# Kernel optimization log

Hardware: AMD Instinct MI355X
Metric: run time of the kernel (lower is better)

## Reference

```python
import jax, jax.numpy as jnp
import numpy as np

B, NQ, NM = 8, 1024, 2048
DIM, HEADS, DHEAD, MLP = 512, 8, 64, 2048
INNER = HEADS * DHEAD
EPS = 1e-5


def layernorm(x, g, b):
    mu = jnp.mean(x, axis=-1, keepdims=True)
    var = jnp.mean(jnp.square(x - mu), axis=-1, keepdims=True)
    return (x - mu) * jax.lax.rsqrt(var + EPS) * g + b


def mha(q_in, k_in, v_in, wq, wk, wv, wo, bo, g, b):
    Bq, Nq, _ = q_in.shape
    Nk = k_in.shape[1]
    q = (q_in @ wq).reshape(Bq, Nq, HEADS, DHEAD)
    k = (k_in @ wk).reshape(Bq, Nk, HEADS, DHEAD)
    v = (v_in @ wv).reshape(Bq, Nk, HEADS, DHEAD)
    scale = DHEAD ** -0.5
    dots = jnp.einsum('bqhd,bkhd->bhqk', q, k) * scale
    attn = jax.nn.softmax(dots, axis=-1)
    out = jnp.einsum('bhqk,bkhd->bqhd', attn, v).reshape(Bq, Nq, INNER)
    out = out @ wo + bo
    return layernorm(out, g, b) + q_in


def ffn(x, w1, b1, w2, b2, g, b):
    h = jax.nn.relu(x @ w1 + b1)
    return layernorm(h @ w2 + b2, g, b) + x


def _mha_params(key, s=0.02):
    ks = jax.random.split(key, 4)
    return dict(
        wq=jax.random.normal(ks[0], (DIM, INNER), jnp.float32) * s,
        wk=jax.random.normal(ks[1], (DIM, INNER), jnp.float32) * s,
        wv=jax.random.normal(ks[2], (DIM, INNER), jnp.float32) * s,
        wo=jax.random.normal(ks[3], (INNER, DIM), jnp.float32) * s,
        bo=jnp.zeros((DIM,), jnp.float32),
        g=jnp.ones((DIM,), jnp.float32),
        b=jnp.zeros((DIM,), jnp.float32),
    )


def _ffn_params(key, s=0.02):
    ks = jax.random.split(key, 2)
    return dict(
        w1=jax.random.normal(ks[0], (DIM, MLP), jnp.float32) * s,
        b1=jnp.zeros((MLP,), jnp.float32),
        w2=jax.random.normal(ks[1], (MLP, DIM), jnp.float32) * s,
        b2=jnp.zeros((DIM,), jnp.float32),
        g=jnp.ones((DIM,), jnp.float32),
        b=jnp.zeros((DIM,), jnp.float32),
    )


def setup_inputs() -> dict:
    key = jax.random.key(0)
    ks = jax.random.split(key, 8)
    inp = {
        'tgt': jax.random.normal(ks[0], (B, NQ, DIM), jnp.float32),
        'memory': jax.random.normal(ks[1], (B, NM, DIM), jnp.float32),
        'pos': jax.random.normal(ks[2], (B, NM, DIM), jnp.float32),
        'query_pos': jax.random.normal(ks[3], (B, NQ, DIM), jnp.float32),
    }
    a0 = _mha_params(ks[4]); f0 = _ffn_params(ks[5])
    a1 = _mha_params(ks[6]); f1 = _ffn_params(ks[7])
    for name, d in (('a0', a0), ('f0', f0), ('a1', a1), ('f1', f1)):
        for k, v in d.items():
            inp[f'{name}_{k}'] = v
    return inp


def reference(tgt, memory, pos, query_pos,
              a0_wq, a0_wk, a0_wv, a0_wo, a0_bo, a0_g, a0_b,
              f0_w1, f0_b1, f0_w2, f0_b2, f0_g, f0_b,
              a1_wq, a1_wk, a1_wv, a1_wo, a1_bo, a1_g, a1_b,
              f1_w1, f1_b1, f1_w2, f1_b2, f1_g, f1_b):
    # self-attention: q=k=tgt+query_pos, v=tgt
    q0 = tgt + query_pos
    x = mha(q0, q0, tgt, a0_wq, a0_wk, a0_wv, a0_wo, a0_bo, a0_g, a0_b)
    x = ffn(x, f0_w1, f0_b1, f0_w2, f0_b2, f0_g, f0_b)
    # cross-attention: q=x+query_pos, k=memory+pos, v=memory
    q = x + query_pos
    k = memory + pos
    x = mha(q, k, memory, a1_wq, a1_wk, a1_wv, a1_wo, a1_bo, a1_g, a1_b)
    x = ffn(x, f1_w1, f1_b1, f1_w2, f1_b2, f1_g, f1_b)
    return x
```

## Files before the change

### kernel.cpp

```cpp
#include <hip/hip_runtime.h>
#include <stdint.h>
#include <stddef.h>

typedef __attribute__((ext_vector_type(8))) short short8;
typedef __attribute__((ext_vector_type(4))) short short4v;
typedef __attribute__((ext_vector_type(4))) float floatx4;

#define DEV __device__ __forceinline__

DEV float bf2f(short s) {
    union { float f; uint32_t u; } v;
    v.u = ((uint32_t)(uint16_t)s) << 16;
    return v.f;
}
DEV short f2bf(float f) {
    union { float f; uint32_t u; } v;
    v.f = f;
    uint32_t u = v.u + 0x7FFFu + ((v.u >> 16) & 1u);
    return (short)(u >> 16);
}
DEV short f2bf_tr(float f) {
    union { float f; uint32_t u; } v;
    v.f = f;
    return (short)(v.u >> 16);
}

template<int BIAS, int RELU, int OUTBF>
__global__ __launch_bounds__(256) void gemm_bt(
    const short* __restrict__ A, const short* __restrict__ Bt,
    const float* __restrict__ bias, void* __restrict__ Cout,
    int M, int N, int K)
{
    __shared__ short Alds[2][128 * 32];
    __shared__ short Blds[2][128 * 32];
    const int tid  = threadIdx.x;
    const int wave = tid >> 6, lane = tid & 63;
    const int g = lane >> 4, li = lane & 15;

    const int gx = gridDim.x;
    int flat = blockIdx.y * gx + blockIdx.x;
    const int nwg = gx * gridDim.y;
    flat = (flat & 7) * (nwg >> 3) + (flat >> 3);
    const long bm = (long)(flat % gx) * 128;
    const long bn = (long)(flat / gx) * 128;

    const int wr = (wave >> 1) * 64;
    const int wc = (wave & 1) * 64;
    const int srow = wave * 32 + (lane >> 2);
    const int scol = (lane & 3) * 8;
    const short* Ap = A + (bm + srow) * (long)K + scol;
    const short* Bp = Bt + (bn + srow) * (long)K + scol;

    auto STAGE = [&](int buf, int k0) {
        __builtin_amdgcn_global_load_lds(
            (const __attribute__((address_space(1))) void*)(Ap + k0),
            (__attribute__((address_space(3))) void*)(&Alds[buf][wave * 1024]), 16, 0, 0);
        __builtin_amdgcn_global_load_lds(
            (const __attribute__((address_space(1))) void*)(Ap + (long)16 * K + k0),
            (__attribute__((address_space(3))) void*)(&Alds[buf][wave * 1024 + 512]), 16, 0, 0);
        __builtin_amdgcn_global_load_lds(
            (const __attribute__((address_space(1))) void*)(Bp + k0),
            (__attribute__((address_space(3))) void*)(&Blds[buf][wave * 1024]), 16, 0, 0);
        __builtin_amdgcn_global_load_lds(
            (const __attribute__((address_space(1))) void*)(Bp + (long)16 * K + k0),
            (__attribute__((address_space(3))) void*)(&Blds[buf][wave * 1024 + 512]), 16, 0, 0);
    };

    floatx4 acc[4][4];
#pragma unroll
    for (int i = 0; i < 4; i++)
#pragma unroll
        for (int j = 0; j < 4; j++) acc[i][j] = (floatx4){0.f, 0.f, 0.f, 0.f};

    STAGE(0, 0);
    __syncthreads();
    int cur = 0;
    for (int k0 = 0; k0 < K; k0 += 32) {
        if (k0 + 32 < K) STAGE(cur ^ 1, k0 + 32);

        short8 af[4], bfr[4];
#pragma unroll
        for (int mi = 0; mi < 4; mi++)
            af[mi] = *(const short8*)(&Alds[cur][(wr + mi * 16 + li) * 32 + g * 8]);
#pragma unroll
        for (int ni = 0; ni < 4; ni++)
            bfr[ni] = *(const short8*)(&Blds[cur][(wc + ni * 16 + li) * 32 + g * 8]);
#pragma unroll
        for (int mi = 0; mi < 4; mi++)
#pragma unroll
            for (int ni = 0; ni < 4; ni++)
                acc[mi][ni] = __builtin_amdgcn_mfma_f32_16x16x32_bf16(
                    af[mi], bfr[ni], acc[mi][ni], 0, 0, 0);

        __syncthreads();
        cur ^= 1;
    }

    float* Cf = (float*)Cout;
    short* Cb = (short*)Cout;
#pragma unroll
    for (int mi = 0; mi < 4; mi++) {
#pragma unroll
        for (int ni = 0; ni < 4; ni++) {
            const long col = bn + wc + ni * 16 + li;
            const float bv = BIAS ? bias[col] : 0.f;
#pragma unroll
            for (int i = 0; i < 4; i++) {
                const long row = bm + wr + mi * 16 + g * 4 + i;
                float v = acc[mi][ni][i] + bv;
                if (RELU) v = fmaxf(v, 0.f);
                if (OUTBF) Cb[row * N + col] = f2bf(v);
                else       Cf[row * N + col] = v;
            }
        }
    }
}

__global__ __launch_bounds__(256) void gemm_bt2(
    const short* __restrict__ A0, const short* __restrict__ A1,
    const short* __restrict__ Bt, short* __restrict__ Cout,
    int M, int N, int K, int nsplit)
{
    __shared__ short Alds[2][128 * 32];
    __shared__ short Blds[2][128 * 32];
    const int tid  = threadIdx.x;
    const int wave = tid >> 6, lane = tid & 63;
    const int g = lane >> 4, li = lane & 15;

    const int gx = gridDim.x;
    int flat = blockIdx.y * gx + blockIdx.x;
    const int nwg = gx * gridDim.y;
    flat = (flat & 7) * (nwg >> 3) + (flat >> 3);
    const long bm = (long)(flat % gx) * 128;
    const long bn = (long)(flat / gx) * 128;

    const int wr = (wave >> 1) * 64;
    const int wc = (wave & 1) * 64;
    const int srow = wave * 32 + (lane >> 2);
    const int scol = (lane & 3) * 8;
    const short* A = (bn < nsplit) ? A0 : A1;
    const short* Ap = A + (bm + srow) * (long)K + scol;
    const short* Bp = Bt + (bn + srow) * (long)K + scol;

    auto STAGE = [&](int buf, int k0) {
        __builtin_amdgcn_global_load_lds(
            (const __attribute__((address_space(1))) void*)(Ap + k0),
            (__attribute__((address_space(3))) void*)(&Alds[buf][wave * 1024]), 16, 0, 0);
        __builtin_amdgcn_global_load_lds(
            (const __attribute__((address_space(1))) void*)(Ap + (long)16 * K + k0),
            (__attribute__((address_space(3))) void*)(&Alds[buf][wave * 1024 + 512]), 16, 0, 0);
        __builtin_amdgcn_global_load_lds(
            (const __attribute__((address_space(1))) void*)(Bp + k0),
            (__attribute__((address_space(3))) void*)(&Blds[buf][wave * 1024]), 16, 0, 0);
        __builtin_amdgcn_global_load_lds(
            (const __attribute__((address_space(1))) void*)(Bp + (long)16 * K + k0),
            (__attribute__((address_space(3))) void*)(&Blds[buf][wave * 1024 + 512]), 16, 0, 0);
    };

    floatx4 acc[4][4];
#pragma unroll
    for (int i = 0; i < 4; i++)
#pragma unroll
        for (int j = 0; j < 4; j++) acc[i][j] = (floatx4){0.f, 0.f, 0.f, 0.f};

    STAGE(0, 0);
    __syncthreads();
    int cur = 0;
    for (int k0 = 0; k0 < K; k0 += 32) {
        if (k0 + 32 < K) STAGE(cur ^ 1, k0 + 32);
        short8 af[4], bfr[4];
#pragma unroll
        for (int mi = 0; mi < 4; mi++)
            af[mi] = *(const short8*)(&Alds[cur][(wr + mi * 16 + li) * 32 + g * 8]);
#pragma unroll
        for (int ni = 0; ni < 4; ni++)
            bfr[ni] = *(const short8*)(&Blds[cur][(wc + ni * 16 + li) * 32 + g * 8]);
#pragma unroll
        for (int mi = 0; mi < 4; mi++)
#pragma unroll
            for (int ni = 0; ni < 4; ni++)
                acc[mi][ni] = __builtin_amdgcn_mfma_f32_16x16x32_bf16(
                    af[mi], bfr[ni], acc[mi][ni], 0, 0, 0);
        __syncthreads();
        cur ^= 1;
    }

#pragma unroll
    for (int mi = 0; mi < 4; mi++)
#pragma unroll
        for (int ni = 0; ni < 4; ni++) {
            const long col = bn + wc + ni * 16 + li;
#pragma unroll
            for (int i = 0; i < 4; i++) {
                const long row = bm + wr + mi * 16 + g * 4 + i;
                Cout[row * N + col] = f2bf(acc[mi][ni][i]);
            }
        }
}

template<int BIAS>
__global__ __launch_bounds__(256) void gemm_bt_sk(
    const short* __restrict__ A, const short* __restrict__ Bt,
    const float* __restrict__ bias, float* __restrict__ Cout,
    int M, int N, int K)
{
    __shared__ short Alds[2][128 * 32];
    __shared__ short Blds[2][128 * 32];
    const int tid  = threadIdx.x;
    const int wave = tid >> 6, lane = tid & 63;
    const int g = lane >> 4, li = lane & 15;
    const int z = blockIdx.z;
    const int Kh = K >> 1;

    const int gx = gridDim.x;
    int flat = blockIdx.y * gx + blockIdx.x;
    const int nwg = gx * gridDim.y;
    flat = (flat & 7) * (nwg >> 3) + (flat >> 3);
    const long bm = (long)(flat % gx) * 128;
    const long bn = (long)(flat / gx) * 128;

    const int wr = (wave >> 1) * 64;
    const int wc = (wave & 1) * 64;
    const int srow = wave * 32 + (lane >> 2);
    const int scol = (lane & 3) * 8;
    const short* Ap = A + (bm + srow) * (long)K + scol + (long)z * Kh;
    const short* Bp = Bt + (bn + srow) * (long)K + scol + (long)z * Kh;
    float* C = Cout + (long)z * M * N;

    auto STAGE = [&](int buf, int k0) {
        __builtin_amdgcn_global_load_lds(
            (const __attribute__((address_space(1))) void*)(Ap + k0),
            (__attribute__((address_space(3))) void*)(&Alds[buf][wave * 1024]), 16, 0, 0);
        __builtin_amdgcn_global_load_lds(
            (const __attribute__((address_space(1))) void*)(Ap + (long)16 * K + k0),
            (__attribute__((address_space(3))) void*)(&Alds[buf][wave * 1024 + 512]), 16, 0, 0);
        __builtin_amdgcn_global_load_lds(
            (const __attribute__((address_space(1))) void*)(Bp + k0),
            (__attribute__((address_space(3))) void*)(&Blds[buf][wave * 1024]), 16, 0, 0);
        __builtin_amdgcn_global_load_lds(
            (const __attribute__((address_space(1))) void*)(Bp + (long)16 * K + k0),
            (__attribute__((address_space(3))) void*)(&Blds[buf][wave * 1024 + 512]), 16, 0, 0);
    };

    floatx4 acc[4][4];
#pragma unroll
    for (int i = 0; i < 4; i++)
#pragma unroll
        for (int j = 0; j < 4; j++) acc[i][j] = (floatx4){0.f, 0.f, 0.f, 0.f};

    STAGE(0, 0);
    __syncthreads();
    int cur = 0;
    for (int k0 = 0; k0 < Kh; k0 += 32) {
        if (k0 + 32 < Kh) STAGE(cur ^ 1, k0 + 32);
        short8 af[4], bfr[4];
#pragma unroll
        for (int mi = 0; mi < 4; mi++)
            af[mi] = *(const short8*)(&Alds[cur][(wr + mi * 16 + li) * 32 + g * 8]);
#pragma unroll
        for (int ni = 0; ni < 4; ni++)
            bfr[ni] = *(const short8*)(&Blds[cur][(wc + ni * 16 + li) * 32 + g * 8]);
#pragma unroll
        for (int mi = 0; mi < 4; mi++)
#pragma unroll
            for (int ni = 0; ni < 4; ni++)
                acc[mi][ni] = __builtin_amdgcn_mfma_f32_16x16x32_bf16(
                    af[mi], bfr[ni], acc[mi][ni], 0, 0, 0);
        __syncthreads();
        cur ^= 1;
    }

#pragma unroll
    for (int mi = 0; mi < 4; mi++)
#pragma unroll
        for (int ni = 0; ni < 4; ni++) {
            const long col = bn + wc + ni * 16 + li;
            const float bv = (BIAS && z == 0) ? bias[col] : 0.f;
#pragma unroll
            for (int i = 0; i < 4; i++) {
                const long row = bm + wr + mi * 16 + g * 4 + i;
                C[row * N + col] = acc[mi][ni][i] + bv;
            }
        }
}

__global__ __launch_bounds__(256) void attn_kernel(
    const short* __restrict__ Qg, const short* __restrict__ Kg,
    const short* __restrict__ VTg, short* __restrict__ Og,
    int NQ, int NK, int ldq, int ldk)
{
    constexpr int LD = 68, LDP = 36;
    __shared__ short Klds[32 * LD];
    __shared__ short Vlds[64 * LD];
    __shared__ short Plds[4][16 * LDP];

    const int tid = threadIdx.x;
    const int wave = tid >> 6, lane = tid & 63;
    const int g = lane >> 4, li = lane & 15;

    const int nqb = NQ >> 6;
    const int i   = blockIdx.x;
    const int xcd = i & 7;
    const int t   = i >> 3;
    const int c   = t % nqb;
    const int gh  = t / nqb;
    const int grp = xcd + 8 * gh;
    const int b   = grp >> 3, h = grp & 7;
    const int q0  = c * 64 + wave * 16;

    const short* qptr = Qg + ((long)(b * NQ + q0 + li) * ldq + h * 64);
    short8 qf[2];
#pragma unroll
    for (int f = 0; f < 2; f++) {
        short8 tq = *(const short8*)(qptr + f * 32 + g * 8);
#pragma unroll
        for (int ii = 0; ii < 8; ii++) tq[ii] = f2bf(bf2f(tq[ii]) * 0.18033688011112042f);
        qf[f] = tq;
    }

    floatx4 acc[4];
#pragma unroll
    for (int s = 0; s < 4; s++) acc[s] = (floatx4){0.f, 0.f, 0.f, 0.f};
    float lsum = 0.f;

    const int skey = tid >> 3, sdc = (tid & 7) * 8;
    const int svd = tid >> 2, svk = (tid & 3) * 8;
    const short* kp = Kg + (long)b * NK * ldk + h * 64 + (long)skey * ldk + sdc;
    const short* vp = VTg + ((long)(b * 512 + h * 64 + svd)) * NK + svk;

    short8 kreg = *(const short8*)kp;  kp += (long)32 * ldk;
    short8 vreg = *(const short8*)vp;  vp += 32;

    for (int kt = 0; kt < NK; kt += 32) {
        __syncthreads();
        *(short8*)(Klds + skey * LD + sdc) = kreg;
        *(short8*)(Vlds + svd * LD + svk) = vreg;
        __syncthreads();
        if (kt + 32 < NK) {
            kreg = *(const short8*)kp;  kp += (long)32 * ldk;
            vreg = *(const short8*)vp;  vp += 32;
        }

        floatx4 sT0 = (floatx4){0.f, 0.f, 0.f, 0.f};
        floatx4 sT1 = (floatx4){0.f, 0.f, 0.f, 0.f};
        {
            short8 k00 = *(const short8*)(Klds + li * LD + g * 8);
            short8 k01 = *(const short8*)(Klds + li * LD + 32 + g * 8);
            short8 k10 = *(const short8*)(Klds + (16 + li) * LD + g * 8);
            short8 k11 = *(const short8*)(Klds + (16 + li) * LD + 32 + g * 8);
            sT0 = __builtin_amdgcn_mfma_f32_16x16x32_bf16(k00, qf[0], sT0, 0, 0, 0);
            sT0 = __builtin_amdgcn_mfma_f32_16x16x32_bf16(k01, qf[1], sT0, 0, 0, 0);
            sT1 = __builtin_amdgcn_mfma_f32_16x16x32_bf16(k10, qf[0], sT1, 0, 0, 0);
            sT1 = __builtin_amdgcn_mfma_f32_16x16x32_bf16(k11, qf[1], sT1, 0, 0, 0);
        }

        const float p0 = exp2f(sT0[0]), p1 = exp2f(sT0[1]);
        const float p2 = exp2f(sT0[2]), p3 = exp2f(sT0[3]);
        const float p4 = exp2f(sT1[0]), p5 = exp2f(sT1[1]);
        const float p6 = exp2f(sT1[2]), p7 = exp2f(sT1[3]);
        lsum += ((p0 + p1) + (p2 + p3)) + ((p4 + p5) + (p6 + p7));

        short4v pw0 = { f2bf_tr(p0), f2bf_tr(p1), f2bf_tr(p2), f2bf_tr(p3) };
        short4v pw1 = { f2bf_tr(p4), f2bf_tr(p5), f2bf_tr(p6), f2bf_tr(p7) };
        *(short4v*)(Plds[wave] + li * LDP + g * 4) = pw0;
        *(short4v*)(Plds[wave] + li * LDP + 16 + g * 4) = pw1;
        short8 pf = *(const short8*)(Plds[wave] + li * LDP + g * 8);

#pragma unroll
        for (int s = 0; s < 4; s++) {
            short8 vf = *(const short8*)(Vlds + (s * 16 + li) * LD + g * 8);
            acc[s] = __builtin_amdgcn_mfma_f32_16x16x32_bf16(vf, pf, acc[s], 0, 0, 0);
        }
    }

    lsum += __shfl_xor(lsum, 16);
    lsum += __shfl_xor(lsum, 32);
    const float inv = 1.f / lsum;
    short* optr = Og + ((long)(b * NQ + q0 + li) * 512 + h * 64);
#pragma unroll
    for (int s = 0; s < 4; s++) {
        short4v o4 = { f2bf(acc[s][0] * inv), f2bf(acc[s][1] * inv),
                       f2bf(acc[s][2] * inv), f2bf(acc[s][3] * inv) };
        *(short4v*)(optr + s * 16 + g * 4) = o4;
    }
}

__global__ __launch_bounds__(256) void add_conv2(
    const float* __restrict__ a, const float* __restrict__ b,
    float* __restrict__ of, short* __restrict__ ob1, short* __restrict__ ob2)
{
    const long i = (long)(blockIdx.x * 256 + threadIdx.x) * 4;
    const float4 va = *(const float4*)(a + i);
    float4 vs = va;
    if (b) {
        const float4 vb = *(const float4*)(b + i);
        vs.x += vb.x; vs.y += vb.y; vs.z += vb.z; vs.w += vb.w;
    }
    if (of) *(float4*)(of + i) = vs;
    short4v o1 = { f2bf(vs.x), f2bf(vs.y), f2bf(vs.z), f2bf(vs.w) };
    *(short4v*)(ob1 + i) = o1;
    if (ob2) {
        short4v o2 = { f2bf(va.x), f2bf(va.y), f2bf(va.z), f2bf(va.w) };
        *(short4v*)(ob2 + i) = o2;
    }
}

__global__ __launch_bounds__(256) void ln_res_kernel(
    const float* __restrict__ X, const float* __restrict__ X2,
    const float* __restrict__ gam, const float* __restrict__ bet,
    const float* __restrict__ res, const float* __restrict__ postadd,
    float* __restrict__ outF, short* __restrict__ outB)
{
    const int row = blockIdx.x * 4 + (threadIdx.x >> 6);
    const int lane = threadIdx.x & 63;
    const long base = (long)row * 512 + lane * 8;
    float x[8];
    *(float4*)(x) = *(const float4*)(X + base);
    *(float4*)(x + 4) = *(const float4*)(X + base + 4);
    if (X2) {
        float x2[8];
        *(float4*)(x2) = *(const float4*)(X2 + base);
        *(float4*)(x2 + 4) = *(const float4*)(X2 + base + 4);
#pragma unroll
        for (int i = 0; i < 8; i++) x[i] += x2[i];
    }
    float s = x[0] + x[1] + x[2] + x[3] + x[4] + x[5] + x[6] + x[7];
#pragma unroll
    for (int o = 1; o < 64; o <<= 1) s += __shfl_xor(s, o);
    const float mu = s * (1.0f / 512.0f);
    float vs = 0.f;
#pragma unroll
    for (int i = 0; i < 8; i++) { const float d = x[i] - mu; vs += d * d; }
#pragma unroll
    for (int o = 1; o < 64; o <<= 1) vs += __shfl_xor(vs, o);
    const float rs = rsqrtf(vs * (1.0f / 512.0f) + 1e-5f);

    float gv[8], bv[8], rv[8];
    *(float4*)(gv) = *(const float4*)(gam + lane * 8);
    *(float4*)(gv + 4) = *(const float4*)(gam + lane * 8 + 4);
    *(float4*)(bv) = *(const float4*)(bet + lane * 8);
    *(float4*)(bv + 4) = *(const float4*)(bet + lane * 8 + 4);
    *(float4*)(rv) = *(const float4*)(res + base);
    *(float4*)(rv + 4) = *(const float4*)(res + base + 4);

    float y[8];
#pragma unroll
    for (int i = 0; i < 8; i++) y[i] = (x[i] - mu) * rs * gv[i] + bv[i] + rv[i];
    if (postadd) {
        float pv[8];
        *(float4*)(pv) = *(const float4*)(postadd + base);
        *(float4*)(pv + 4) = *(const float4*)(postadd + base + 4);
#pragma unroll
        for (int i = 0; i < 8; i++) y[i] += pv[i];
    }
    *(float4*)(outF + base) = *(float4*)(y);
    *(float4*)(outF + base + 4) = *(float4*)(y + 4);
    if (outB) {
        short8 ob;
#pragma unroll
        for (int i = 0; i < 8; i++) ob[i] = f2bf(y[i]);
        *(short8*)(outB + base) = ob;
    }
}

__global__ __launch_bounds__(256) void wtrans8(
    const float* __restrict__ w0, const float* __restrict__ w1,
    const float* __restrict__ w2, const float* __restrict__ w3,
    const float* __restrict__ w4, const float* __restrict__ w5,
    const float* __restrict__ w6, const float* __restrict__ w7,
    short* __restrict__ o0, short* __restrict__ o1,
    short* __restrict__ o2, short* __restrict__ o3,
    short* __restrict__ o4, short* __restrict__ o5,
    short* __restrict__ o6, short* __restrict__ o7,
    int K, int N)
{
    const float* Ws[8] = {w0, w1, w2, w3, w4, w5, w6, w7};
    short* Os[8] = {o0, o1, o2, o3, o4, o5, o6, o7};
    const float* W = Ws[blockIdx.z];
    short* Wt = Os[blockIdx.z];
    __shared__ short t[32][33];
    const int n0 = blockIdx.x * 32, k0 = blockIdx.y * 32;
    const int tx = threadIdx.x & 31, ty = threadIdx.x >> 5;
    for (int r = ty; r < 32; r += 8)
        t[r][tx] = f2bf(W[(long)(k0 + r) * N + n0 + tx]);
    __syncthreads();
    for (int r = ty; r < 32; r += 8)
        Wt[(long)(n0 + r) * K + k0 + tx] = t[tx][r];
}

__global__ __launch_bounds__(256) void vtrans(
    const short* __restrict__ V, short* __restrict__ VT,
    int NK, int ldv, int voff)
{
    __shared__ short t[32][33];
    const int b = blockIdx.z;
    const int key0 = blockIdx.x * 32, c0 = blockIdx.y * 32;
    const int tx = threadIdx.x & 31, ty = threadIdx.x >> 5;
    for (int r = ty; r < 32; r += 8)
        t[r][tx] = V[((long)b * NK + key0 + r) * ldv + voff + c0 + tx];
    __syncthreads();
    for (int r = ty; r < 32; r += 8)
        VT[((long)b * 512 + c0 + r) * NK + key0 + tx] = t[tx][r];
}

extern "C" void kernel_launch(void* const* d_in, const int* in_sizes, int n_in,
                              void* d_out, int out_size, void* d_ws, size_t ws_size,
                              hipStream_t stream)
{
    (void)in_sizes; (void)n_in; (void)out_size; (void)ws_size;
    const float* tgt   = (const float*)d_in[0];
    const float* mem   = (const float*)d_in[1];
    const float* pos   = (const float*)d_in[2];
    const float* qpos  = (const float*)d_in[3];
    const float* a0_wq = (const float*)d_in[4];
    const float* a0_wk = (const float*)d_in[5];
    const float* a0_wv = (const float*)d_in[6];
    const float* a0_wo = (const float*)d_in[7];
    const float* a0_bo = (const float*)d_in[8];
    const float* a0_g  = (const float*)d_in[9];
    const float* a0_b  = (const float*)d_in[10];
    const float* f0_w1 = (const float*)d_in[11];
    const float* f0_b1 = (const float*)d_in[12];
    const float* f0_w2 = (const float*)d_in[13];
    const float* f0_b2 = (const float*)d_in[14];
    const float* f0_g  = (const float*)d_in[15];
    const float* f0_b  = (const float*)d_in[16];
    const float* a1_wq = (const float*)d_in[17];
    const float* a1_wk = (const float*)d_in[18];
    const float* a1_wv = (const float*)d_in[19];
    const float* a1_wo = (const float*)d_in[20];
    const float* a1_bo = (const float*)d_in[21];
    const float* a1_g  = (const float*)d_in[22];
    const float* a1_b  = (const float*)d_in[23];
    const float* f1_w1 = (const float*)d_in[24];
    const float* f1_b1 = (const float*)d_in[25];
    const float* f1_w2 = (const float*)d_in[26];
    const float* f1_b2 = (const float*)d_in[27];
    const float* f1_g  = (const float*)d_in[28];
    const float* f1_b  = (const float*)d_in[29];

    const int M1 = 8 * 1024;
    const int M2 = 8 * 2048;
    const size_t MB = 1ull << 20;
    char* ws = (char*)d_ws;

    float* resid = (float*)(ws + 0 * MB);
    float* xf    = (float*)(ws + 16 * MB);
    short* xb    = (short*)(ws + 32 * MB);
    short* wb    = (short*)(ws + 40 * MB);
    short* a0_wqt = wb;            short* a0_wkt = wb + 262144;
    short* a0_wvt = wb + 524288;   short* a0_wot = wb + 786432;
    short* f0_w1t = wb + 1048576;  short* f0_w2t = wb + 2097152;
    short* a1_wqt = wb + 3145728;  short* a1_wkt = wb + 3407872;
    short* a1_wvt = wb + 3670016;  short* a1_wot = wb + 3932160;
    short* f1_w1t = wb + 4194304;  short* f1_w2t = wb + 5242880;
    char* S = ws + 56 * MB;

    wtrans8<<<dim3(16, 16, 8), 256, 0, stream>>>(
        a0_wq, a0_wk, a0_wv, a0_wo, a1_wq, a1_wk, a1_wv, a1_wo,
        a0_wqt, a0_wkt, a0_wvt, a0_wot, a1_wqt, a1_wkt, a1_wvt, a1_wot, 512, 512);
    wtrans8<<<dim3(64, 16, 2), 256, 0, stream>>>(
        f0_w1, f1_w1, nullptr, nullptr, nullptr, nullptr, nullptr, nullptr,
        f0_w1t, f1_w1t, nullptr, nullptr, nullptr, nullptr, nullptr, nullptr, 512, 2048);
    wtrans8<<<dim3(16, 64, 2), 256, 0, stream>>>(
        f0_w2, f1_w2, nullptr, nullptr, nullptr, nullptr, nullptr, nullptr,
        f0_w2t, f1_w2t, nullptr, nullptr, nullptr, nullptr, nullptr, nullptr, 2048, 512);

    short* QKVs = (short*)(S + 0 * MB);
    short* VsT  = (short*)(S + 24 * MB);
    short* AOs  = (short*)(S + 32 * MB);
    float* P0a  = (float*)(S + 40 * MB);
    float* P1a  = (float*)(S + 56 * MB);
    short* q0b  = (short*)(S + 72 * MB);
    short* tgtb = (short*)(S + 80 * MB);

    add_conv2<<<4096, 256, 0, stream>>>(tgt, qpos, resid, q0b, tgtb);

    gemm_bt2<<<dim3(64, 12), 256, 0, stream>>>(q0b, tgtb, a0_wqt, QKVs,
                                               M1, 1536, 512, 1024);
    vtrans<<<dim3(32, 16, 8), 256, 0, stream>>>(QKVs, VsT, 1024, 1536, 1024);
    attn_kernel<<<1024, 256, 0, stream>>>(QKVs, QKVs + 512, VsT, AOs,
                                          1024, 1024, 1536, 1536);
    gemm_bt_sk<1><<<dim3(64, 4, 2), 256, 0, stream>>>(AOs, a0_wot, a0_bo, P0a,
                                                      M1, 512, 512);
    ln_res_kernel<<<2048, 256, 0, stream>>>(P0a, P1a, a0_g, a0_b, resid, nullptr, xf, xb);

    short* Hb  = (short*)(S + 0 * MB);
    float* P0f = (float*)(S + 32 * MB);
    float* P1f = (float*)(S + 48 * MB);
    short* qcb = (short*)(S + 88 * MB);
    gemm_bt<1,1,1><<<dim3(64, 16), 256, 0, stream>>>(xb, f0_w1t, f0_b1, Hb, M1, 2048, 512);
    gemm_bt_sk<1><<<dim3(64, 4, 2), 256, 0, stream>>>(Hb, f0_w2t, f0_b2, P0f,
                                                      M1, 512, 2048);
    ln_res_kernel<<<2048, 256, 0, stream>>>(P0f, P1f, f0_g, f0_b, xf, qpos, resid, qcb);

    short* kcb  = (short*)(S + 0 * MB);
    short* memb = (short*)(S + 16 * MB);
    short* KVc  = (short*)(S + 32 * MB);
    float* P0c  = (float*)(S + 32 * MB);
    float* P1c  = (float*)(S + 48 * MB);
    short* VcT  = (short*)(S + 64 * MB);
    short* Qc   = (short*)(S + 80 * MB);
    short* AOc  = (short*)(S + 96 * MB);

    add_conv2<<<8192, 256, 0, stream>>>(mem, pos, nullptr, kcb, memb);

    gemm_bt<0,0,1><<<dim3(64, 4), 256, 0, stream>>>(qcb, a1_wqt, nullptr, Qc, M1, 512, 512);
    gemm_bt2<<<dim3(128, 8), 256, 0, stream>>>(kcb, memb, a1_wkt, KVc,
                                               M2, 1024, 512, 512);
    vtrans<<<dim3(64, 16, 8), 256, 0, stream>>>(KVc, VcT, 2048, 1024, 512);
    attn_kernel<<<1024, 256, 0, stream>>>(Qc, KVc, VcT, AOc,
                                          1024, 2048, 512, 1024);
    gemm_bt_sk<1><<<dim3(64, 4, 2), 256, 0, stream>>>(AOc, a1_wot, a1_bo, P0c,
                                                      M1, 512, 512);
    ln_res_kernel<<<2048, 256, 0, stream>>>(P0c, P1c, a1_g, a1_b, resid, nullptr, xf, xb);

    short* Hb2  = (short*)(S + 0 * MB);
    float* P0g  = (float*)(S + 32 * MB);
    float* P1g  = (float*)(S + 48 * MB);
    gemm_bt<1,1,1><<<dim3(64, 16), 256, 0, stream>>>(xb, f1_w1t, f1_b1, Hb2, M1, 2048, 512);
    gemm_bt_sk<1><<<dim3(64, 4, 2), 256, 0, stream>>>(Hb2, f1_w2t, f1_b2, P0g,
                                                      M1, 512, 2048);
    ln_res_kernel<<<2048, 256, 0, stream>>>(P0g, P1g, f1_g, f1_b, xf, nullptr,
                                            (float*)d_out, nullptr);
}
```

Before: 451.0 us.

## Fuse V transpose into QKV GEMM epilogue and double query rows per attention wave

The QKV/KV projection GEMM now writes the V columns straight into the transposed layout used by attention, so the separate vtrans kernel launches and their extra global round trip go away. The attention kernel now handles 32 query rows per wave (128 per block), so each K/V tile staged in shared memory serves twice as many queries and the grid is halved. The cost is more registers per wave and fewer blocks, which may lower occupancy. Scratch buffer offsets are reshuffled to fit the new layout.

```diff
diff --git a/kernel.cpp b/kernel.cpp
--- a/kernel.cpp
+++ b/kernel.cpp
@@ -116,10 +116,11 @@
     }
 }
 
-__global__ __launch_bounds__(256) void gemm_bt2(
+__global__ __launch_bounds__(256) void gemm_bt2vt(
     const short* __restrict__ A0, const short* __restrict__ A1,
     const short* __restrict__ Bt, short* __restrict__ Cout,
-    int M, int N, int K, int nsplit)
+    short* __restrict__ VT,
+    int M, int N, int K, int nsplit, int ldc, int vtoff, int nkvlog)
 {
     __shared__ short Alds[2][128 * 32];
     __shared__ short Blds[2][128 * 32];
@@ -185,17 +186,34 @@
         cur ^= 1;
     }
 
-#pragma unroll
-    for (int mi = 0; mi < 4; mi++)
-#pragma unroll
-        for (int ni = 0; ni < 4; ni++) {
-            const long col = bn + wc + ni * 16 + li;
-#pragma unroll
-            for (int i = 0; i < 4; i++) {
-                const long row = bm + wr + mi * 16 + g * 4 + i;
-                Cout[row * N + col] = f2bf(acc[mi][ni][i]);
+    if (bn < vtoff) {
+#pragma unroll
+        for (int mi = 0; mi < 4; mi++)
+#pragma unroll
+            for (int ni = 0; ni < 4; ni++) {
+                const long col = bn + wc + ni * 16 + li;
+#pragma unroll
+                for (int i = 0; i < 4; i++) {
+                    const long row = bm + wr + mi * 16 + g * 4 + i;
+                    Cout[row * ldc + col] = f2bf(acc[mi][ni][i]);
+                }
+            }
+    } else {
+        const int mask = (1 << nkvlog) - 1;
+#pragma unroll
+        for (int mi = 0; mi < 4; mi++) {
+            const int row0 = (int)(bm + wr + mi * 16 + g * 4);
+            const int bb = row0 >> nkvlog;
+            const int key0 = row0 & mask;
+#pragma unroll
+            for (int ni = 0; ni < 4; ni++) {
+                const int d = (int)(bn + wc + ni * 16 + li) - vtoff;
+                short4v o = { f2bf(acc[mi][ni][0]), f2bf(acc[mi][ni][1]),
+                              f2bf(acc[mi][ni][2]), f2bf(acc[mi][ni][3]) };
+                *(short4v*)(VT + ((long)(bb * 512 + d) << nkvlog) + key0) = o;
             }
         }
+    }
 }
 
 template<int BIAS>
@@ -292,13 +310,13 @@
     constexpr int LD = 68, LDP = 36;
     __shared__ short Klds[32 * LD];
     __shared__ short Vlds[64 * LD];
-    __shared__ short Plds[4][16 * LDP];
+    __shared__ short Plds[4][32 * LDP];
 
     const int tid = threadIdx.x;
     const int wave = tid >> 6, lane = tid & 63;
     const int g = lane >> 4, li = lane & 15;
 
-    const int nqb = NQ >> 6;
+    const int nqb = NQ >> 7;
     const int i   = blockIdx.x;
     const int xcd = i & 7;
     const int t   = i >> 3;
@@ -306,22 +324,30 @@
     const int gh  = t / nqb;
     const int grp = xcd + 8 * gh;
     const int b   = grp >> 3, h = grp & 7;
-    const int q0  = c * 64 + wave * 16;
-
-    const short* qptr = Qg + ((long)(b * NQ + q0 + li) * ldq + h * 64);
-    short8 qf[2];
+    const int q0  = c * 128 + wave * 32;
+
+    const short* qptrA = Qg + ((long)(b * NQ + q0 + li) * ldq + h * 64);
+    const short* qptrB = qptrA + (long)16 * ldq;
+    short8 qfA[2], qfB[2];
 #pragma unroll
     for (int f = 0; f < 2; f++) {
-        short8 tq = *(const short8*)(qptr + f * 32 + g * 8);
-#pragma unroll
-        for (int ii = 0; ii < 8; ii++) tq[ii] = f2bf(bf2f(tq[ii]) * 0.18033688011112042f);
-        qf[f] = tq;
-    }
-
-    floatx4 acc[4];
-#pragma unroll
-    for (int s = 0; s < 4; s++) acc[s] = (floatx4){0.f, 0.f, 0.f, 0.f};
-    float lsum = 0.f;
+        short8 ta = *(const short8*)(qptrA + f * 32 + g * 8);
+        short8 tb = *(const short8*)(qptrB + f * 32 + g * 8);
+#pragma unroll
+        for (int ii = 0; ii < 8; ii++) {
+            ta[ii] = f2bf(bf2f(ta[ii]) * 0.18033688011112042f);
+            tb[ii] = f2bf(bf2f(tb[ii]) * 0.18033688011112042f);
+        }
+        qfA[f] = ta; qfB[f] = tb;
+    }
+
+    floatx4 accA[4], accB[4];
+#pragma unroll
+    for (int s = 0; s < 4; s++) {
+        accA[s] = (floatx4){0.f, 0.f, 0.f, 0.f};
+        accB[s] = (floatx4){0.f, 0.f, 0.f, 0.f};
+    }
+    float lsumA = 0.f, lsumB = 0.f;
 
     const int skey = tid >> 3, sdc = (tid & 7) * 8;
     const int svd = tid >> 2, svk = (tid & 3) * 8;
@@ -341,47 +367,71 @@
             vreg = *(const short8*)vp;  vp += 32;
         }
 
-        floatx4 sT0 = (floatx4){0.f, 0.f, 0.f, 0.f};
-        floatx4 sT1 = (floatx4){0.f, 0.f, 0.f, 0.f};
+        floatx4 sA0 = (floatx4){0.f, 0.f, 0.f, 0.f};
+        floatx4 sA1 = (floatx4){0.f, 0.f, 0.f, 0.f};
+        floatx4 sB0 = (floatx4){0.f, 0.f, 0.f, 0.f};
+        floatx4 sB1 = (floatx4){0.f, 0.f, 0.f, 0.f};
         {
             short8 k00 = *(const short8*)(Klds + li * LD + g * 8);
             short8 k01 = *(const short8*)(Klds + li * LD + 32 + g * 8);
             short8 k10 = *(const short8*)(Klds + (16 + li) * LD + g * 8);
             short8 k11 = *(const short8*)(Klds + (16 + li) * LD + 32 + g * 8);
-            sT0 = __builtin_amdgcn_mfma_f32_16x16x32_bf16(k00, qf[0], sT0, 0, 0, 0);
-            sT0 = __builtin_amdgcn_mfma_f32_16x16x32_bf16(k01, qf[1], sT0, 0, 0, 0);
-            sT1 = __builtin_amdgcn_mfma_f32_16x16x32_bf16(k10, qf[0], sT1, 0, 0, 0);
-            sT1 = __builtin_amdgcn_mfma_f32_16x16x32_bf16(k11, qf[1], sT1, 0, 0, 0);
+            sA0 = __builtin_amdgcn_mfma_f32_16x16x32_bf16(k00, qfA[0], sA0, 0, 0, 0);
+            sA0 = __builtin_amdgcn_mfma_f32_16x16x32_bf16(k01, qfA[1], sA0, 0, 0, 0);
+            sA1 = __builtin_amdgcn_mfma_f32_16x16x32_bf16(k10, qfA[0], sA1, 0, 0, 0);
+            sA1 = __builtin_amdgcn_mfma_f32_16x16x32_bf16(k11, qfA[1], sA1, 0, 0, 0);
+            sB0 = __builtin_amdgcn_mfma_f32_16x16x32_bf16(k00, qfB[0], sB0, 0, 0, 0);
+            sB0 = __builtin_amdgcn_mfma_f32_16x16x32_bf16(k01, qfB[1], sB0, 0, 0, 0);
+            sB1 = __builtin_amdgcn_mfma_f32_16x16x32_bf16(k10, qfB[0], sB1, 0, 0, 0);
+            sB1 = __builtin_amdgcn_mfma_f32_16x16x32_bf16(k11, qfB[1], sB1, 0, 0, 0);
         }
 
-        const float p0 = exp2f(sT0[0]), p1 = exp2f(sT0[1]);
-        const float p2 = exp2f(sT0[2]), p3 = exp2f(sT0[3]);
-        const float p4 = exp2f(sT1[0]), p5 = exp2f(sT1[1]);
-        const float p6 = exp2f(sT1[2]), p7 = exp2f(sT1[3]);
-        lsum += ((p0 + p1) + (p2 + p3)) + ((p4 + p5) + (p6 + p7));
-
-        short4v pw0 = { f2bf_tr(p0), f2bf_tr(p1), f2bf_tr(p2), f2bf_tr(p3) };
-        short4v pw1 = { f2bf_tr(p4), f2bf_tr(p5), f2bf_tr(p6), f2bf_tr(p7) };
-        *(short4v*)(Plds[wave] + li * LDP + g * 4) = pw0;
-        *(short4v*)(Plds[wave] + li * LDP + 16 + g * 4) = pw1;
-        short8 pf = *(const short8*)(Plds[wave] + li * LDP + g * 8);
+        const float a0 = exp2f(sA0[0]), a1 = exp2f(sA0[1]);
+        const float a2 = exp2f(sA0[2]), a3 = exp2f(sA0[3]);
+        const float a4 = exp2f(sA1[0]), a5 = exp2f(sA1[1]);
+        const float a6 = exp2f(sA1[2]), a7 = exp2f(sA1[3]);
+        lsumA += ((a0 + a1) + (a2 + a3)) + ((a4 + a5) + (a6 + a7));
+        const float b0 = exp2f(sB0[0]), b1 = exp2f(sB0[1]);
+        const float b2 = exp2f(sB0[2]), b3 = exp2f(sB0[3]);
+        const float b4 = exp2f(sB1[0]), b5 = exp2f(sB1[1]);
+        const float b6 = exp2f(sB1[2]), b7 = exp2f(sB1[3]);
+        lsumB += ((b0 + b1) + (b2 + b3)) + ((b4 + b5) + (b6 + b7));
+
+        short4v pa0 = { f2bf_tr(a0), f2bf_tr(a1), f2bf_tr(a2), f2bf_tr(a3) };
+        short4v pa1 = { f2bf_tr(a4), f2bf_tr(a5), f2bf_tr(a6), f2bf_tr(a7) };
+        short4v pb0 = { f2bf_tr(b0), f2bf_tr(b1), f2bf_tr(b2), f2bf_tr(b3) };
+        short4v pb1 = { f2bf_tr(b4), f2bf_tr(b5), f2bf_tr(b6), f2bf_tr(b7) };
+        *(short4v*)(Plds[wave] + li * LDP + g * 4) = pa0;
+        *(short4v*)(Plds[wave] + li * LDP + 16 + g * 4) = pa1;
+        *(short4v*)(Plds[wave] + (16 + li) * LDP + g * 4) = pb0;
+        *(short4v*)(Plds[wave] + (16 + li) * LDP + 16 + g * 4) = pb1;
+        short8 pfA = *(const short8*)(Plds[wave] + li * LDP + g * 8);
+        short8 pfB = *(const short8*)(Plds[wave] + (16 + li) * LDP + g * 8);
 
 #pragma unroll
         for (int s = 0; s < 4; s++) {
             short8 vf = *(const short8*)(Vlds + (s * 16 + li) * LD + g * 8);
-            acc[s] = __builtin_amdgcn_mfma_f32_16x16x32_bf16(vf, pf, acc[s], 0, 0, 0);
+            accA[s] = __builtin_amdgcn_mfma_f32_16x16x32_bf16(vf, pfA, accA[s], 0, 0, 0);
+            accB[s] = __builtin_amdgcn_mfma_f32_16x16x32_bf16(vf, pfB, accB[s], 0, 0, 0);
         }
     }
 
-    lsum += __shfl_xor(lsum, 16);
-    lsum += __shfl_xor(lsum, 32);
-    const float inv = 1.f / lsum;
-    short* optr = Og + ((long)(b * NQ + q0 + li) * 512 + h * 64);
+    lsumA += __shfl_xor(lsumA, 16);
+    lsumA += __shfl_xor(lsumA, 32);
+    lsumB += __shfl_xor(lsumB, 16);
+    lsumB += __shfl_xor(lsumB, 32);
+    const float invA = 1.f / lsumA;
+    const float invB = 1.f / lsumB;
+    short* optrA = Og + ((long)(b * NQ + q0 + li) * 512 + h * 64);
+    short* optrB = optrA + (long)16 * 512;
 #pragma unroll
     for (int s = 0; s < 4; s++) {
-        short4v o4 = { f2bf(acc[s][0] * inv), f2bf(acc[s][1] * inv),
-                       f2bf(acc[s][2] * inv), f2bf(acc[s][3] * inv) };
-        *(short4v*)(optr + s * 16 + g * 4) = o4;
+        short4v oa = { f2bf(accA[s][0] * invA), f2bf(accA[s][1] * invA),
+                       f2bf(accA[s][2] * invA), f2bf(accA[s][3] * invA) };
+        short4v ob = { f2bf(accB[s][0] * invB), f2bf(accB[s][1] * invB),
+                       f2bf(accB[s][2] * invB), f2bf(accB[s][3] * invB) };
+        *(short4v*)(optrA + s * 16 + g * 4) = oa;
+        *(short4v*)(optrB + s * 16 + g * 4) = ob;
     }
 }
 
@@ -486,21 +536,6 @@
     __syncthreads();
     for (int r = ty; r < 32; r += 8)
         Wt[(long)(n0 + r) * K + k0 + tx] = t[tx][r];
-}
-
-__global__ __launch_bounds__(256) void vtrans(
-    const short* __restrict__ V, short* __restrict__ VT,
-    int NK, int ldv, int voff)
-{
-    __shared__ short t[32][33];
-    const int b = blockIdx.z;
-    const int key0 = blockIdx.x * 32, c0 = blockIdx.y * 32;
-    const int tx = threadIdx.x & 31, ty = threadIdx.x >> 5;
-    for (int r = ty; r < 32; r += 8)
-        t[r][tx] = V[((long)b * NK + key0 + r) * ldv + voff + c0 + tx];
-    __syncthreads();
-    for (int r = ty; r < 32; r += 8)
-        VT[((long)b * 512 + c0 + r) * NK + key0 + tx] = t[tx][r];
 }
 
 extern "C" void kernel_launch(void* const* d_in, const int* in_sizes, int n_in,
@@ -566,21 +601,20 @@
         f0_w2, f1_w2, nullptr, nullptr, nullptr, nullptr, nullptr, nullptr,
         f0_w2t, f1_w2t, nullptr, nullptr, nullptr, nullptr, nullptr, nullptr, 2048, 512);
 
-    short* QKVs = (short*)(S + 0 * MB);
-    short* VsT  = (short*)(S + 24 * MB);
-    short* AOs  = (short*)(S + 32 * MB);
-    float* P0a  = (float*)(S + 40 * MB);
-    float* P1a  = (float*)(S + 56 * MB);
-    short* q0b  = (short*)(S + 72 * MB);
-    short* tgtb = (short*)(S + 80 * MB);
+    short* QKs  = (short*)(S + 0 * MB);
+    short* VsT  = (short*)(S + 16 * MB);
+    short* AOs  = (short*)(S + 24 * MB);
+    float* P0a  = (float*)(S + 32 * MB);
+    float* P1a  = (float*)(S + 48 * MB);
+    short* q0b  = (short*)(S + 64 * MB);
+    short* tgtb = (short*)(S + 72 * MB);
 
     add_conv2<<<4096, 256, 0, stream>>>(tgt, qpos, resid, q0b, tgtb);
 
-    gemm_bt2<<<dim3(64, 12), 256, 0, stream>>>(q0b, tgtb, a0_wqt, QKVs,
-                                               M1, 1536, 512, 1024);
-    vtrans<<<dim3(32, 16, 8), 256, 0, stream>>>(QKVs, VsT, 1024, 1536, 1024);
-    attn_kernel<<<1024, 256, 0, stream>>>(QKVs, QKVs + 512, VsT, AOs,
-                                          1024, 1024, 1536, 1536);
+    gemm_bt2vt<<<dim3(64, 12), 256, 0, stream>>>(q0b, tgtb, a0_wqt, QKs, VsT,
+                                                 M1, 1536, 512, 1024, 1024, 1024, 10);
+    attn_kernel<<<512, 256, 0, stream>>>(QKs, QKs + 512, VsT, AOs,
+                                         1024, 1024, 1024, 1024);
     gemm_bt_sk<1><<<dim3(64, 4, 2), 256, 0, stream>>>(AOs, a0_wot, a0_bo, P0a,
                                                       M1, 512, 512);
     ln_res_kernel<<<2048, 256, 0, stream>>>(P0a, P1a, a0_g, a0_b, resid, nullptr, xf, xb);
@@ -588,7 +622,7 @@
     short* Hb  = (short*)(S + 0 * MB);
     float* P0f = (float*)(S + 32 * MB);
     float* P1f = (float*)(S + 48 * MB);
-    short* qcb = (short*)(S + 88 * MB);
+    short* qcb = (short*)(S + 80 * MB);
     gemm_bt<1,1,1><<<dim3(64, 16), 256, 0, stream>>>(xb, f0_w1t, f0_b1, Hb, M1, 2048, 512);
     gemm_bt_sk<1><<<dim3(64, 4, 2), 256, 0, stream>>>(Hb, f0_w2t, f0_b2, P0f,
                                                       M1, 512, 2048);
@@ -596,21 +630,20 @@
 
     short* kcb  = (short*)(S + 0 * MB);
     short* memb = (short*)(S + 16 * MB);
-    short* KVc  = (short*)(S + 32 * MB);
+    short* Kc   = (short*)(S + 32 * MB);
+    short* VcT  = (short*)(S + 48 * MB);
+    short* Qc   = (short*)(S + 64 * MB);
+    short* AOc  = (short*)(S + 72 * MB);
     float* P0c  = (float*)(S + 32 * MB);
     float* P1c  = (float*)(S + 48 * MB);
-    short* VcT  = (short*)(S + 64 * MB);
-    short* Qc   = (short*)(S + 80 * MB);
-    short* AOc  = (short*)(S + 96 * MB);
 
     add_conv2<<<8192, 256, 0, stream>>>(mem, pos, nullptr, kcb, memb);
 
     gemm_bt<0,0,1><<<dim3(64, 4), 256, 0, stream>>>(qcb, a1_wqt, nullptr, Qc, M1, 512, 512);
-    gemm_bt2<<<dim3(128, 8), 256, 0, stream>>>(kcb, memb, a1_wkt, KVc,
-                                               M2, 1024, 512, 512);
-    vtrans<<<dim3(64, 16, 8), 256, 0, stream>>>(KVc, VcT, 2048, 1024, 512);
-    attn_kernel<<<1024, 256, 0, stream>>>(Qc, KVc, VcT, AOc,
-                                          1024, 2048, 512, 1024);
+    gemm_bt2vt<<<dim3(128, 8), 256, 0, stream>>>(kcb, memb, a1_wkt, Kc, VcT,
+                                                 M2, 1024, 512, 512, 512, 512, 11);
+    attn_kernel<<<512, 256, 0, stream>>>(Qc, Kc, VcT, AOc,
+                                         1024, 2048, 512, 512);
     gemm_bt_sk<1><<<dim3(64, 4, 2), 256, 0, stream>>>(AOc, a1_wot, a1_bo, P0c,
                                                       M1, 512, 512);
     ln_res_kernel<<<2048, 256, 0, stream>>>(P0c, P1c, a1_g, a1_b, resid, nullptr, xf, xb);
```

Result: faster. 432.5 us (median of 2 runs) (-4.1%).
